# Optimization experiments

Measured on AMD Instinct MI355X. Metric: run time of the kernel, lower is better.

The kernel has to match this reference:

```python
import jax, jax.numpy as jnp
import numpy as np

D_MODEL = 1024
D_STATE = 16
EXPANSION = 2
GROUPS = 16
D_INNER = EXPANSION * D_MODEL          # 2048
GROUP_SIZE = D_INNER // GROUPS         # 128
B, T = 2, 1024


def _rmsnorm(x, g, eps=1e-6):
    return x * jax.lax.rsqrt(jnp.mean(x * x, axis=-1, keepdims=True) + eps) * g


def setup_inputs() -> dict:
    key = jax.random.key(0)
    ks = jax.random.split(key, 8)
    s_in = 1.0 / np.sqrt(D_MODEL)
    s_inner = 1.0 / np.sqrt(D_INNER)
    s_ff = 1.0 / np.sqrt(4 * D_MODEL)
    return {
        "x": jax.random.normal(ks[0], (B, T, D_MODEL), dtype=jnp.float32),
        "A_log": jnp.log(jnp.linspace(1.0, float(D_STATE), D_STATE)).astype(jnp.float32),
        "g1": jnp.ones((D_MODEL,), jnp.float32),
        "g2": jnp.ones((D_MODEL,), jnp.float32),
        "W_in": jax.random.normal(ks[1], (2 * D_INNER, D_MODEL), jnp.float32) * s_in,
        "W_param": jax.random.normal(ks[2], (GROUPS * (1 + 2 * D_STATE), D_INNER), jnp.float32) * s_inner,
        "W_out": jax.random.normal(ks[3], (D_MODEL, D_INNER), jnp.float32) * s_inner,
        "W_ffn1": jax.random.normal(ks[4], (4 * D_MODEL, D_MODEL), jnp.float32) * s_in,
        "b_ffn1": jnp.zeros((4 * D_MODEL,), jnp.float32),
        "W_ffn2": jax.random.normal(ks[5], (D_MODEL, 4 * D_MODEL), jnp.float32) * s_ff,
        "b_ffn2": jnp.zeros((D_MODEL,), jnp.float32),
    }


def _ssm(u, delta, b, c, A_log):
    # u,delta: [B,T,D]; b,c: [B,T,D,N]. Sequential recurrence equivalent to
    # the module's chunked cumprod/cumsum formulation.
    A = -jnp.exp(A_log)                                   # [N]
    deltaA = jnp.clip(delta[..., None] * A, -10.0, 10.0)  # [B,T,D,N]
    expA = jnp.exp(deltaA)
    frac_exact = (expA - 1.0) / (A + 1e-12)
    frac = jnp.where(jnp.abs(deltaA) < 1e-4, delta[..., None], frac_exact)
    Bu = frac * (b * u[..., None])                        # [B,T,D,N]

    def step(h, inp):
        Ah_t, Bu_t, c_t = inp                             # [B,D,N] each
        h = Ah_t * h + Bu_t
        return h, jnp.sum(h * c_t, axis=-1)               # y_t: [B,D]

    tm = lambda a: jnp.moveaxis(a, 1, 0)                  # time-major [T,B,D,N]
    h0 = jnp.zeros(u.shape[:1] + u.shape[2:] + (A.shape[0],), u.dtype)
    _, ys = jax.lax.scan(step, h0, (tm(expA), tm(Bu), tm(c)))
    return jnp.moveaxis(ys, 0, 1)                         # [B,T,D]


def reference(x, A_log, g1, g2, W_in, W_param, W_out, W_ffn1, b_ffn1, W_ffn2, b_ffn2):
    Bsz, Tlen, _ = x.shape
    z = _rmsnorm(x, g1)
    xz_gate = jnp.einsum('btd,ed->bte', z, W_in)          # [B,T,2*D_inner]
    xz, gate = jnp.split(xz_gate, 2, axis=-1)
    xz = jax.nn.silu(xz)

    params = jnp.einsum('btd,pd->btp', xz, W_param)
    params = params.reshape(Bsz, Tlen, GROUPS, 1 + 2 * D_STATE)
    delta_g = params[..., :1]                             # [B,T,G,1]
    b_g = params[..., 1:1 + D_STATE]                      # [B,T,G,N]
    c_g = params[..., 1 + D_STATE:]                       # [B,T,G,N]
    delta = jax.nn.softplus(jnp.repeat(delta_g[..., 0], GROUP_SIZE, axis=2))  # [B,T,D_inner]
    b = jnp.repeat(b_g, GROUP_SIZE, axis=2)               # [B,T,D_inner,N]
    c = jnp.repeat(c_g, GROUP_SIZE, axis=2)

    y_ssm = _ssm(xz, delta, b, c, A_log)                  # [B,T,D_inner]
    y = y_ssm * jax.nn.silu(gate)
    y = jnp.einsum('bte,de->btd', y, W_out)
    x = x + y                                             # residual (dropout/droppath = identity in eval)

    h2 = _rmsnorm(x, g2)
    ffn = jnp.einsum('btf,df->btd',
                     jax.nn.silu(jnp.einsum('btd,fd->btf', h2, W_ffn1) + b_ffn1),
                     W_ffn2) + b_ffn2
    return x + ffn
```

## Files before the change

kernel.cpp:

```cpp
#include <hip/hip_runtime.h>
#include <hip/hip_bf16.h>
#include <stdint.h>

#define ROWS 2048
#define DM   1024
#define DI   2048
#define PPAD 640

typedef __bf16 bf16_t;
typedef __attribute__((ext_vector_type(8))) __bf16 bf16x8;
typedef __attribute__((ext_vector_type(4))) __bf16 bf16x4;
typedef __attribute__((ext_vector_type(4))) float f32x4;
typedef __attribute__((address_space(1))) void gvoid_t;
typedef __attribute__((address_space(3))) void lvoid_t;

#define G_IN   1048576ll
#define G_PAR  327680ll
#define G_OUT  524288ll
#define G_F1   1048576ll
#define G_F2   1048576ll
__global__ __launch_bounds__(256) void cvt_all(const float* __restrict__ W_in,
                                               const float* __restrict__ W_param,
                                               const float* __restrict__ W_out,
                                               const float* __restrict__ W_f1,
                                               const float* __restrict__ W_f2,
                                               bf16_t* o_in, bf16_t* o_par,
                                               bf16_t* o_out, bf16_t* o_f1,
                                               bf16_t* o_f2) {
  int64_t g4 = (int64_t)blockIdx.x * 256 + threadIdx.x;
  const float* src; bf16_t* dst; int64_t e;
  if (g4 < G_IN) { e = g4 * 4; src = W_in; dst = o_in; }
  else if (g4 < G_IN + G_PAR) {
    e = (g4 - G_IN) * 4;
    int row = (int)(e >> 11), col = (int)(e & 2047);
    float4 v = make_float4(0.f, 0.f, 0.f, 0.f);
    if (row < 528) v = *(const float4*)(W_param + (int64_t)row * 2048 + col);
    bf16_t* o = o_par + e;
    o[0] = (bf16_t)v.x; o[1] = (bf16_t)v.y; o[2] = (bf16_t)v.z; o[3] = (bf16_t)v.w;
    return;
  }
  else if (g4 < G_IN + G_PAR + G_OUT) { e = (g4 - G_IN - G_PAR) * 4; src = W_out; dst = o_out; }
  else if (g4 < G_IN + G_PAR + G_OUT + G_F1) { e = (g4 - G_IN - G_PAR - G_OUT) * 4; src = W_f1; dst = o_f1; }
  else { e = (g4 - G_IN - G_PAR - G_OUT - G_F1) * 4; src = W_f2; dst = o_f2; }
  float4 v = *(const float4*)(src + e);
  bf16_t* o = dst + e;
  o[0] = (bf16_t)v.x; o[1] = (bf16_t)v.y; o[2] = (bf16_t)v.z; o[3] = (bf16_t)v.w;
}

__global__ __launch_bounds__(256) void rmsnorm_k(const float* __restrict__ x,
                                                 const float* __restrict__ g,
                                                 bf16_t* __restrict__ out) {
  int row = blockIdx.x;
  int tid = threadIdx.x;
  const float4 v = *(const float4*)(x + (int64_t)row * DM + tid * 4);
  float ss = v.x * v.x + v.y * v.y + v.z * v.z + v.w * v.w;
#pragma unroll
  for (int o = 32; o; o >>= 1) ss += __shfl_xor(ss, o, 64);
  __shared__ float red[4];
  if ((tid & 63) == 0) red[tid >> 6] = ss;
  __syncthreads();
  float tot = red[0] + red[1] + red[2] + red[3];
  float sc = rsqrtf(tot * (1.0f / DM) + 1e-6f);
  const float4 gv = *(const float4*)(g + tid * 4);
  bf16_t* o = out + (int64_t)row * DM + tid * 4;
  o[0] = (bf16_t)(v.x * sc * gv.x);
  o[1] = (bf16_t)(v.y * sc * gv.y);
  o[2] = (bf16_t)(v.z * sc * gv.z);
  o[3] = (bf16_t)(v.w * sc * gv.w);
}

__global__ __launch_bounds__(256) void silu_cvt(const float* __restrict__ in,
                                                bf16_t* __restrict__ out,
                                                int in_stride, int ncols) {
  int64_t e = ((int64_t)blockIdx.x * 256 + threadIdx.x) * 4;
  int row = (int)(e / ncols);
  int col = (int)(e % ncols);
  const float4 v = *(const float4*)(in + (int64_t)row * in_stride + col);
  bf16_t* o = out + e;
  o[0] = (bf16_t)(v.x / (1.f + expf(-v.x)));
  o[1] = (bf16_t)(v.y / (1.f + expf(-v.y)));
  o[2] = (bf16_t)(v.z / (1.f + expf(-v.z)));
  o[3] = (bf16_t)(v.w / (1.f + expf(-v.w)));
}

__global__ __launch_bounds__(256) void ssm_prep(const float* __restrict__ params,
                                                const float* __restrict__ A_log,
                                                float* __restrict__ ssmp, int nparts) {
  int gid = blockIdx.x * 256 + threadIdx.x;
  int bg = gid >> 10, t = gid & 1023;
  int b = bg >> 4, g = bg & 15;
  float acc[33];
#pragma unroll
  for (int i = 0; i < 33; ++i) acc[i] = 0.f;
  for (int p = 0; p < nparts; ++p) {
    const float* pr = params + (int64_t)p * ROWS * PPAD + (int64_t)(b * 1024 + t) * PPAD + g * 33;
#pragma unroll
    for (int i = 0; i < 33; ++i) acc[i] += pr[i];
  }
  float raw = acc[0];
  float delta = raw > 0.f ? raw + log1pf(expf(-raw)) : log1pf(expf(raw));
  float* o = ssmp + (int64_t)gid * 48;
#pragma unroll
  for (int s = 0; s < 16; ++s) {
    float A = -expf(A_log[s]);
    float dA = delta * A;
    dA = fminf(10.f, fmaxf(-10.f, dA));
    float e = expf(dA);
    float frac = (fabsf(dA) < 1e-4f) ? delta : (e - 1.f) / (A + 1e-12f);
    o[s] = dA;
    o[16 + s] = frac * acc[1 + s];
    o[32 + s] = acc[17 + s];
  }
}

__global__ __launch_bounds__(256) void reduce_rms(const bf16_t* __restrict__ P,
                                                  const float* __restrict__ x,
                                                  const float* __restrict__ g,
                                                  float* __restrict__ xmid,
                                                  bf16_t* __restrict__ zb) {
  int row = blockIdx.x;
  int tid = threadIdx.x;
  int64_t base = (int64_t)row * DM + tid * 4;
  float4 v = *(const float4*)(x + base);
#pragma unroll
  for (int p = 0; p < 4; ++p) {
    bf16x4 pv = *(const bf16x4*)(P + (int64_t)p * ROWS * DM + base);
    v.x += (float)pv[0]; v.y += (float)pv[1]; v.z += (float)pv[2]; v.w += (float)pv[3];
  }
  *(float4*)(xmid + base) = v;
  float ss = v.x * v.x + v.y * v.y + v.z * v.z + v.w * v.w;
#pragma unroll
  for (int o = 32; o; o >>= 1) ss += __shfl_xor(ss, o, 64);
  __shared__ float red[4];
  if ((tid & 63) == 0) red[tid >> 6] = ss;
  __syncthreads();
  float tot = red[0] + red[1] + red[2] + red[3];
  float sc = rsqrtf(tot * (1.0f / DM) + 1e-6f);
  const float4 gv = *(const float4*)(g + tid * 4);
  bf16_t* o = zb + base;
  o[0] = (bf16_t)(v.x * sc * gv.x);
  o[1] = (bf16_t)(v.y * sc * gv.y);
  o[2] = (bf16_t)(v.z * sc * gv.z);
  o[3] = (bf16_t)(v.w * sc * gv.w);
}

__global__ __launch_bounds__(256) void reduce_bias(const bf16_t* __restrict__ P,
                                                   const float* __restrict__ res,
                                                   const float* __restrict__ bias,
                                                   float* __restrict__ out) {
  int64_t e = ((int64_t)blockIdx.x * 256 + threadIdx.x) * 4;
  int col = (int)(e % DM);
  float4 v = *(const float4*)(res + e);
  const float4 bv = *(const float4*)(bias + col);
  v.x += bv.x; v.y += bv.y; v.z += bv.z; v.w += bv.w;
#pragma unroll
  for (int p = 0; p < 4; ++p) {
    bf16x4 pv = *(const bf16x4*)(P + (int64_t)p * ROWS * DM + e);
    v.x += (float)pv[0]; v.y += (float)pv[1]; v.z += (float)pv[2]; v.w += (float)pv[3];
  }
  *(float4*)(out + e) = v;
}


__global__ __launch_bounds__(256) void ssm_chunk(const float* __restrict__ ssmp,
                                                 const bf16_t* __restrict__ u,
                                                 float* __restrict__ S,
                                                 float* __restrict__ Etot) {
  __shared__ __align__(16) float cf[64 * 48];
  __shared__ __align__(16) float Lb[64 * 16];
  __shared__ __align__(16) bf16_t wl[16 * 64];
  __shared__ __align__(16) bf16_t Ut[128 * 64];
  int bgc = blockIdx.x;
  int bg = bgc >> 4, c = bgc & 15;
  int b = bg >> 4, g = bg & 15;
  int t0 = c * 64;
  int tid = threadIdx.x;
  {
    const float4* src = (const float4*)(ssmp + ((int64_t)bg * 1024 + t0) * 48);
    float4* dst = (float4*)cf;
#pragma unroll
    for (int i = 0; i < 3; ++i) dst[i * 256 + tid] = src[i * 256 + tid];
  }
  {
    int lt = tid >> 4;
    int c8 = (tid & 15) * 8;
#pragma unroll
    for (int p = 0; p < 4; ++p) {
      int t = p * 16 + lt;
      bf16x8 v = *(const bf16x8*)(u + ((int64_t)(b * 1024) + t0 + t) * 2048 + g * 128 + c8);
#pragma unroll
      for (int j = 0; j < 8; ++j)
        Ut[(c8 + j) * 64 + (((t >> 3) ^ j) << 3) + (t & 7)] = v[j];
    }
  }
  __syncthreads();
  if (tid < 16) {
    float l = 0.f;
    for (int t = 0; t < 64; ++t) { l += cf[t * 48 + tid]; Lb[t * 16 + tid] = l; }
  }
  __syncthreads();
  {
    int s = tid >> 4, tb4 = (tid & 15) * 4;
    float lend = Lb[63 * 16 + s];
    bf16x4 wv;
#pragma unroll
    for (int j = 0; j < 4; ++j) {
      int t = tb4 + j;
      wv[j] = (bf16_t)(__expf(lend - Lb[t * 16 + s]) * cf[t * 48 + 16 + s]);
    }
    unsigned byo = (unsigned)(s * 128 + tb4 * 2) ^ ((unsigned)(s & 7) << 4);
    *(bf16x4*)((char*)wl + byo) = wv;
    if (tid < 16) Etot[(int64_t)bgc * 16 + tid] = __expf(Lb[63 * 16 + tid]);
  }
  __syncthreads();
  {
    int lane = tid & 63, wave = tid >> 6;
    int fr = lane & 15, kq = lane >> 4;
    f32x4 acc2[2] = {};
#pragma unroll
    for (int kk = 0; kk < 2; ++kk) {
      int kb = kk * 4 + kq;
      bf16x8 af = *(const bf16x8*)((const char*)wl +
                    ((unsigned)(fr * 128 + kb * 16) ^ ((unsigned)(fr & 7) << 4)));
#pragma unroll
      for (int q = 0; q < 2; ++q) {
        int ch = (wave * 2 + q) * 16 + fr;
        bf16x8 bfr = *(const bf16x8*)((const char*)Ut +
                       ((unsigned)(ch * 128 + kb * 16) ^ ((unsigned)(ch & 7) << 4)));
        acc2[q] = __builtin_amdgcn_mfma_f32_16x16x32_bf16(af, bfr, acc2[q], 0, 0, 0);
      }
    }
    float* Sp = S + (int64_t)bgc * 2048;
#pragma unroll
    for (int q = 0; q < 2; ++q) {
      int ch = (wave * 2 + q) * 16 + fr;
#pragma unroll
      for (int j = 0; j < 4; ++j) Sp[(kq * 4 + j) * 128 + ch] = acc2[q][j];
    }
  }
}

__global__ __launch_bounds__(256) void ssm_combine(const float* __restrict__ S,
                                                   const float* __restrict__ Etot,
                                                   float* __restrict__ H) {
  int gid = blockIdx.x * 256 + threadIdx.x;
  int bg = gid >> 11;
  int s = (gid >> 7) & 15;
  int ch = gid & 127;
  float h = 0.f;
  for (int c = 0; c < 16; ++c) {
    int bgc = bg * 16 + c;
    int64_t idx = ((int64_t)bgc * 16 + s) * 128 + ch;
    H[idx] = h;
    h = Etot[(int64_t)bgc * 16 + s] * h + S[idx];
  }
}

template <int GM>
__global__ __launch_bounds__(256) void ssm_out(const float* __restrict__ ssmp,
                                               const bf16_t* __restrict__ u,
                                               const float* __restrict__ H,
                                               const float* __restrict__ gate_f,
                                               const bf16_t* __restrict__ gate_b,
                                               int gstride,
                                               bf16_t* __restrict__ yout) {
  __shared__ __align__(16) float cf[64 * 48];
  __shared__ __align__(16) float Lb[64 * 16];
  __shared__ __align__(16) bf16_t Km[64 * 64];
  __shared__ __align__(16) bf16_t Ut[128 * 64];
  __shared__ __align__(16) bf16_t Hb[128 * 32];
  int bgc = blockIdx.x;
  int bg = bgc >> 4, c = bgc & 15;
  int b = bg >> 4, g = bg & 15;
  int t0 = c * 64;
  int tid = threadIdx.x;
  int lane = tid & 63, wave = tid >> 6;
  {
    const float4* src = (const float4*)(ssmp + ((int64_t)bg * 1024 + t0) * 48);
    float4* dst = (float4*)cf;
#pragma unroll
    for (int i = 0; i < 3; ++i) dst[i * 256 + tid] = src[i * 256 + tid];
  }
  {
    int lt = tid >> 4;
    int c8 = (tid & 15) * 8;
#pragma unroll
    for (int p = 0; p < 4; ++p) {
      int t = p * 16 + lt;
      bf16x8 v = *(const bf16x8*)(u + ((int64_t)(b * 1024) + t0 + t) * 2048 + g * 128 + c8);
#pragma unroll
      for (int j = 0; j < 8; ++j)
        Ut[(c8 + j) * 64 + (((t >> 3) ^ j) << 3) + (t & 7)] = v[j];
    }
  }
  {
    int ch = tid >> 1, h8 = (tid & 1) * 8;
    const float* Hp = H + (int64_t)bgc * 2048 + ch;
#pragma unroll
    for (int j = 0; j < 8; ++j) {
      Hb[ch * 32 + h8 + j] = (bf16_t)Hp[(h8 + j) * 128];
      Hb[ch * 32 + 16 + h8 + j] = (bf16_t)0.f;
    }
  }
  __syncthreads();
  if (tid < 16) {
    float l = 0.f;
    for (int t = 0; t < 64; ++t) { l += cf[t * 48 + tid]; Lb[t * 16 + tid] = l; }
  }
  __syncthreads();
  {
    int t = tid >> 2, tp0 = (tid & 3) * 16;
    float4 cv[4], lv[4];
#pragma unroll
    for (int i = 0; i < 4; ++i) {
      cv[i] = *(const float4*)&cf[t * 48 + 32 + i * 4];
      lv[i] = *(const float4*)&Lb[t * 16 + i * 4];
    }
    float kv[16];
#pragma unroll
    for (int i = 0; i < 16; ++i) {
      int tp = tp0 + i;
      float k = 0.f;
      if (tp <= t) {
#pragma unroll
        for (int q = 0; q < 4; ++q) {
          float4 lpv = *(const float4*)&Lb[tp * 16 + q * 4];
          float4 fbv = *(const float4*)&cf[tp * 48 + 16 + q * 4];
          k += cv[q].x * __expf(lv[q].x - lpv.x) * fbv.x
             + cv[q].y * __expf(lv[q].y - lpv.y) * fbv.y
             + cv[q].z * __expf(lv[q].z - lpv.z) * fbv.z
             + cv[q].w * __expf(lv[q].w - lpv.w) * fbv.w;
        }
      }
      kv[i] = k;
    }
    bf16x8 lo, hi;
#pragma unroll
    for (int i = 0; i < 8; ++i) { lo[i] = (bf16_t)kv[i]; hi[i] = (bf16_t)kv[8 + i]; }
    unsigned b0 = (unsigned)(t * 128 + tp0 * 2) ^ ((unsigned)(t & 7) << 4);
    unsigned b1 = (unsigned)(t * 128 + tp0 * 2 + 16) ^ ((unsigned)(t & 7) << 4);
    *(bf16x8*)((char*)Km + b0) = lo;
    *(bf16x8*)((char*)Km + b1) = hi;
  }
  __syncthreads();
  int fr = lane & 15, kq = lane >> 4;
  int trow = (wave >> 1) * 32, wc = (wave & 1) * 64;
  f32x4 acc[2][4] = {};
#pragma unroll
  for (int kk = 0; kk < 2; ++kk) {
    int kb = kk * 4 + kq;
    bf16x8 af[2];
#pragma unroll
    for (int mi = 0; mi < 2; ++mi) {
      int row = trow + mi * 16 + fr;
      af[mi] = *(const bf16x8*)((const char*)Km +
                 ((unsigned)(row * 128 + kb * 16) ^ ((unsigned)(row & 7) << 4)));
    }
#pragma unroll
    for (int ni = 0; ni < 4; ++ni) {
      int ch = wc + ni * 16 + fr;
      bf16x8 bfr = *(const bf16x8*)((const char*)Ut +
                     ((unsigned)(ch * 128 + kb * 16) ^ ((unsigned)(ch & 7) << 4)));
#pragma unroll
      for (int mi = 0; mi < 2; ++mi)
        acc[mi][ni] = __builtin_amdgcn_mfma_f32_16x16x32_bf16(af[mi], bfr, acc[mi][ni], 0, 0, 0);
    }
  }
  {
    int s0 = kq * 8;
    bf16x8 cef[2];
    if (s0 < 16) {
#pragma unroll
      for (int mi = 0; mi < 2; ++mi) {
        int t = trow + mi * 16 + fr;
#pragma unroll
        for (int j = 0; j < 8; ++j)
          cef[mi][j] = (bf16_t)(cf[t * 48 + 32 + s0 + j] * __expf(Lb[t * 16 + s0 + j]));
      }
    } else {
#pragma unroll
      for (int mi = 0; mi < 2; ++mi)
#pragma unroll
        for (int j = 0; j < 8; ++j) cef[mi][j] = (bf16_t)0.f;
    }
#pragma unroll
    for (int ni = 0; ni < 4; ++ni) {
      int ch = wc + ni * 16 + fr;
      bf16x8 bhf = *(const bf16x8*)((const char*)Hb + ch * 64 + s0 * 2);
#pragma unroll
      for (int mi = 0; mi < 2; ++mi)
        acc[mi][ni] = __builtin_amdgcn_mfma_f32_16x16x32_bf16(cef[mi], bhf, acc[mi][ni], 0, 0, 0);
    }
  }
  {
    int64_t rowbase = (int64_t)b * 1024 + t0;
    int colbase = g * 128;
#pragma unroll
    for (int mi = 0; mi < 2; ++mi) {
#pragma unroll
      for (int ni = 0; ni < 4; ++ni) {
        int col = colbase + wc + ni * 16 + fr;
#pragma unroll
        for (int j = 0; j < 4; ++j) {
          int t = trow + mi * 16 + kq * 4 + j;
          float sg;
          if (GM) {
            sg = (float)gate_b[(rowbase + t) * 2048 + col];
          } else {
            float gv = gate_f[(rowbase + t) * (int64_t)gstride + col];
            sg = gv / (1.f + __expf(-gv));
          }
          yout[(rowbase + t) * 2048 + col] = (bf16_t)(acc[mi][ni][j] * sg);
        }
      }
    }
  }
}

template <int EPI>
__device__ __forceinline__ void epi_store(float v, int64_t r, int64_t cn, int N,
                                          float* Cz, const float* bias,
                                          const float* res, bf16_t* obf,
                                          bf16_t* ogate, int z) {
  if (EPI & 1) v += bias[cn];
  if (EPI & 2) v += res[r * N + cn];
  if (EPI & 4) {
    float sv = v / (1.f + __expf(-v));
    if (cn < 2048) obf[r * 2048 + cn] = (bf16_t)sv;
    else ogate[r * 2048 + cn - 2048] = (bf16_t)sv;
  } else if (EPI & 8) {
    obf[r * N + cn] = (bf16_t)(v / (1.f + __expf(-v)));
  } else if (EPI & 16) {
    obf[(int64_t)z * ROWS * N + r * N + cn] = (bf16_t)v;
  } else {
    Cz[r * N + cn] = v;
  }
}

template <int EPI>
__global__ __launch_bounds__(256) void gemm_bt(const bf16_t* __restrict__ A,
                                               const bf16_t* __restrict__ Bw,
                                               float* __restrict__ C,
                                               const float* __restrict__ bias,
                                               const float* __restrict__ res,
                                               bf16_t* __restrict__ obf,
                                               bf16_t* __restrict__ ogate,
                                               int N, int Kps) {
  __shared__ bf16_t As[2][128 * 64];
  __shared__ bf16_t Bs[2][128 * 64];
  const int tid = threadIdx.x;
  const int wave = tid >> 6;
  const int lane = tid & 63;
  const int64_t m0 = (int64_t)blockIdx.y * 128;
  const int64_t n0 = (int64_t)blockIdx.x * 128;
  const int K = Kps * gridDim.z;
  const int kbeg = blockIdx.z * Kps;
  float* Cz = C + (int64_t)blockIdx.z * ROWS * N;
  const int wm = (wave >> 1) * 64;
  const int wn = (wave & 1) * 64;
  f32x4 acc[4][4] = {};

  const int er = tid >> 3;
  const int ec = (tid * 8) & 63;
  const int fr = lane & 15;
  const int kq = (lane >> 4) * 8;

  auto stage = [&](int buf, int k0) {
#pragma unroll
    for (int i = 0; i < 4; ++i) {
      const bf16_t* ga = A + (m0 + er + i * 32) * K + k0 + ec;
      __builtin_amdgcn_global_load_lds((gvoid_t*)ga,
                                       (lvoid_t*)&As[buf][(i * 256 + wave * 64) * 8],
                                       16, 0, 0);
    }
#pragma unroll
    for (int i = 0; i < 4; ++i) {
      const bf16_t* gb = Bw + (n0 + er + i * 32) * K + k0 + ec;
      __builtin_amdgcn_global_load_lds((gvoid_t*)gb,
                                       (lvoid_t*)&Bs[buf][(i * 256 + wave * 64) * 8],
                                       16, 0, 0);
    }
  };
  auto compute = [&](int buf) {
#pragma unroll
    for (int kk = 0; kk < 2; ++kk) {
      bf16x8 af[4], bv[4];
#pragma unroll
      for (int mi = 0; mi < 4; ++mi)
        af[mi] = *reinterpret_cast<const bf16x8*>(&As[buf][(wm + mi * 16 + fr) * 64 + kk * 32 + kq]);
#pragma unroll
      for (int ni = 0; ni < 4; ++ni)
        bv[ni] = *reinterpret_cast<const bf16x8*>(&Bs[buf][(wn + ni * 16 + fr) * 64 + kk * 32 + kq]);
#pragma unroll
      for (int mi = 0; mi < 4; ++mi)
#pragma unroll
        for (int ni = 0; ni < 4; ++ni)
          acc[mi][ni] = __builtin_amdgcn_mfma_f32_16x16x32_bf16(af[mi], bv[ni], acc[mi][ni], 0, 0, 0);
    }
  };

  const int nk = Kps >> 6;
  stage(0, kbeg);
  asm volatile("s_waitcnt vmcnt(0)" ::: "memory");
  __builtin_amdgcn_s_barrier();
  int kc = kbeg;
  for (int t = 0; t < nk; t += 2) {
    stage(1, kc + 64);
    compute(0);
    asm volatile("s_waitcnt vmcnt(0)" ::: "memory");
    __builtin_amdgcn_s_barrier();
    if (t + 2 < nk) stage(0, kc + 128);
    compute(1);
    asm volatile("s_waitcnt vmcnt(0)" ::: "memory");
    __builtin_amdgcn_s_barrier();
    kc += 128;
  }

  const int crow = (lane >> 4) * 4;
  const int ccol = lane & 15;
#pragma unroll
  for (int mi = 0; mi < 4; ++mi)
#pragma unroll
    for (int ni = 0; ni < 4; ++ni)
#pragma unroll
      for (int j = 0; j < 4; ++j)
        epi_store<EPI>(acc[mi][ni][j], m0 + wm + mi * 16 + crow + j,
                       n0 + wn + ni * 16 + ccol, N, Cz, bias, res, obf, ogate,
                       blockIdx.z);
}

template <int EPI>
__global__ __launch_bounds__(512, 2) void gemm_big(const bf16_t* __restrict__ A,
                                                   const bf16_t* __restrict__ Bw,
                                                   float* __restrict__ C,
                                                   const float* __restrict__ bias,
                                                   const float* __restrict__ res,
                                                   bf16_t* __restrict__ obf,
                                                   bf16_t* __restrict__ ogate,
                                                   int N, int Kps) {
  __shared__ bf16_t As[2][128 * 64];
  __shared__ bf16_t Bs[2][256 * 64];
  const int tid = threadIdx.x;
  const int wave = tid >> 6;
  const int lane = tid & 63;
  const int64_t m0 = (int64_t)blockIdx.y * 128;
  const int64_t n0 = (int64_t)blockIdx.x * 256;
  const int K = Kps * gridDim.z;
  const int kbeg = blockIdx.z * Kps;
  float* Cz = C + (int64_t)blockIdx.z * ROWS * N;
  const int wm = (wave >> 2) * 64;
  const int wc = (wave & 3) * 64;
  const int fr = lane & 15;
  const int kq16 = (lane >> 4) * 16;
  const int er = tid >> 3;
  const int ec_sw = ((tid & 7) * 8) ^ ((er & 7) << 3);
  f32x4 acc[4][4] = {};

  auto stage = [&](int buf, int k0) {
#pragma unroll
    for (int i = 0; i < 2; ++i) {
      const bf16_t* ga = A + (m0 + er + i * 64) * K + k0 + ec_sw;
      __builtin_amdgcn_global_load_lds((gvoid_t*)ga,
          (lvoid_t*)((char*)&As[buf][0] + i * 8192 + wave * 1024), 16, 0, 0);
    }
#pragma unroll
    for (int i = 0; i < 4; ++i) {
      const bf16_t* gb = Bw + (n0 + er + i * 64) * K + k0 + ec_sw;
      __builtin_amdgcn_global_load_lds((gvoid_t*)gb,
          (lvoid_t*)((char*)&Bs[buf][0] + i * 8192 + wave * 1024), 16, 0, 0);
    }
  };

  const int nk = Kps >> 6;
  stage(0, kbeg);
  if (nk > 1) {
    stage(1, kbeg + 64);
    asm volatile("s_waitcnt vmcnt(6)" ::: "memory");
  } else {
    asm volatile("s_waitcnt vmcnt(0)" ::: "memory");
  }
  __builtin_amdgcn_s_barrier();
  __builtin_amdgcn_sched_barrier(0);

  for (int t = 0; t < nk; ++t) {
    const int buf = t & 1;
    bf16x8 af[2][4], bf[2][4];
#pragma unroll
    for (int kk = 0; kk < 2; ++kk) {
#pragma unroll
      for (int mi = 0; mi < 4; ++mi) {
        int r = wm + mi * 16 + fr;
        af[kk][mi] = *(const bf16x8*)((const char*)&As[buf][0] + r * 128 +
                       ((kk * 64 + kq16) ^ ((r & 7) << 4)));
      }
#pragma unroll
      for (int ni = 0; ni < 4; ++ni) {
        int r = wc + ni * 16 + fr;
        bf[kk][ni] = *(const bf16x8*)((const char*)&Bs[buf][0] + r * 128 +
                       ((kk * 64 + kq16) ^ ((r & 7) << 4)));
      }
    }
    asm volatile("s_waitcnt lgkmcnt(0)" ::: "memory");
    __builtin_amdgcn_sched_barrier(0);
    __builtin_amdgcn_s_barrier();
    __builtin_amdgcn_sched_barrier(0);
    if (t + 2 < nk) stage(buf, kbeg + (t + 2) * 64);
    __builtin_amdgcn_s_setprio(1);
#pragma unroll
    for (int kk = 0; kk < 2; ++kk)
#pragma unroll
      for (int mi = 0; mi < 4; ++mi)
#pragma unroll
        for (int ni = 0; ni < 4; ++ni)
          acc[mi][ni] = __builtin_amdgcn_mfma_f32_16x16x32_bf16(
              af[kk][mi], bf[kk][ni], acc[mi][ni], 0, 0, 0);
    __builtin_amdgcn_s_setprio(0);
    if (t + 1 < nk) {
      if (t + 2 < nk) asm volatile("s_waitcnt vmcnt(6)" ::: "memory");
      else            asm volatile("s_waitcnt vmcnt(0)" ::: "memory");
      __builtin_amdgcn_s_barrier();
      __builtin_amdgcn_sched_barrier(0);
    }
  }

  const int crow = (lane >> 4) * 4;
  const int ccol = lane & 15;
#pragma unroll
  for (int mi = 0; mi < 4; ++mi)
#pragma unroll
    for (int ni = 0; ni < 4; ++ni)
#pragma unroll
      for (int j = 0; j < 4; ++j)
        epi_store<EPI>(acc[mi][ni][j], m0 + wm + mi * 16 + crow + j,
                       n0 + wc + ni * 16 + ccol, N, Cz, bias, res, obf, ogate,
                       blockIdx.z);
}

extern "C" void kernel_launch(void* const* d_in, const int* in_sizes, int n_in,
                              void* d_out, int out_size, void* d_ws, size_t ws_size,
                              hipStream_t stream) {
  const float* x       = (const float*)d_in[0];
  const float* A_log   = (const float*)d_in[1];
  const float* g1      = (const float*)d_in[2];
  const float* g2      = (const float*)d_in[3];
  const float* W_in    = (const float*)d_in[4];
  const float* W_param = (const float*)d_in[5];
  const float* W_out   = (const float*)d_in[6];
  const float* W_ffn1  = (const float*)d_in[7];
  const float* b_ffn1  = (const float*)d_in[8];
  const float* W_ffn2  = (const float*)d_in[9];
  const float* b_ffn2  = (const float*)d_in[10];
  float* out = (float*)d_out;

  char* ws = (char*)d_ws;
  size_t off = 0;
  auto alloc = [&](size_t bytes) {
    char* p = ws + off;
    off += (bytes + 255) & ~(size_t)255;
    return p;
  };
  bf16_t* wb_in  = (bf16_t*)alloc(4096ull * 1024 * 2);
  bf16_t* wb_par = (bf16_t*)alloc((size_t)PPAD * 2048 * 2);
  bf16_t* wb_out = (bf16_t*)alloc(1024ull * 2048 * 2);
  bf16_t* wb_f1  = (bf16_t*)alloc(4096ull * 1024 * 2);
  bf16_t* wb_f2  = (bf16_t*)alloc(1024ull * 4096 * 2);
  bf16_t* zbuf   = (bf16_t*)alloc(2048ull * 1024 * 2);
  float*  xzg    = (float*)alloc(2048ull * 4096 * 4);
  float*  params = (float*)alloc(2048ull * PPAD * 4);
  float*  ssmp   = (float*)alloc(32ull * 1024 * 48 * 4);
  float*  xmid   = (float*)alloc(2048ull * 1024 * 4);
  char*   regA   = alloc(2048ull * 4096 * 2);
  bf16_t* xz_act = (bf16_t*)regA;
  bf16_t* y_b16  = (bf16_t*)(regA + 2048ull * 2048 * 2);
  bf16_t* f_act  = (bf16_t*)regA;
  bf16_t* sgate  = (bf16_t*)xzg;
  float* Sbuf = params;
  float* Etot = params + 32ull * 16 * 16 * 128;
  float* Hbuf = xmid;
  float*  psum = (float*)alloc(4ull * ROWS * 1024 * 4);
  bf16_t* pb16 = (bf16_t*)psum;
  const bool sk = (off <= ws_size);

  dim3 b256(256), b512(512);
  cvt_all<<<15616, b256, 0, stream>>>(W_in, W_param, W_out, W_ffn1, W_ffn2,
                                      wb_in, wb_par, wb_out, wb_f1, wb_f2);
  rmsnorm_k<<<2048, b256, 0, stream>>>(x, g1, zbuf);

  if (sk) {
    gemm_big<4><<<dim3(16, 16), b512, 0, stream>>>(zbuf, wb_in, psum, nullptr, nullptr, xz_act, sgate, 4096, 1024);
    gemm_bt<0><<<dim3(PPAD / 128, 16, 4), b256, 0, stream>>>(xz_act, wb_par, psum, nullptr, nullptr, nullptr, nullptr, PPAD, 512);
    ssm_prep<<<128, b256, 0, stream>>>(psum, A_log, ssmp, 4);
    ssm_chunk<<<512, b256, 0, stream>>>(ssmp, xz_act, Sbuf, Etot);
    ssm_combine<<<256, b256, 0, stream>>>(Sbuf, Etot, Hbuf);
    ssm_out<1><<<512, b256, 0, stream>>>(ssmp, xz_act, Hbuf, nullptr, sgate, 2048, y_b16);
    gemm_big<16><<<dim3(4, 16, 4), b512, 0, stream>>>(y_b16, wb_out, psum, nullptr, nullptr, pb16, nullptr, 1024, 512);
    reduce_rms<<<2048, b256, 0, stream>>>(pb16, x, g2, xmid, zbuf);
    gemm_big<9><<<dim3(16, 16), b512, 0, stream>>>(zbuf, wb_f1, psum, b_ffn1, nullptr, f_act, nullptr, 4096, 1024);
    gemm_big<16><<<dim3(4, 16, 4), b512, 0, stream>>>(f_act, wb_f2, psum, nullptr, nullptr, pb16, nullptr, 1024, 1024);
    reduce_bias<<<2048, b256, 0, stream>>>(pb16, xmid, b_ffn2, out);
  } else {
    gemm_bt<0><<<dim3(32, 16), b256, 0, stream>>>(zbuf, wb_in, xzg, nullptr, nullptr, nullptr, nullptr, 4096, 1024);
    silu_cvt<<<4096, b256, 0, stream>>>(xzg, xz_act, 4096, 2048);
    gemm_bt<0><<<dim3(PPAD / 128, 16), b256, 0, stream>>>(xz_act, wb_par, params, nullptr, nullptr, nullptr, nullptr, PPAD, 2048);
    ssm_prep<<<128, b256, 0, stream>>>(params, A_log, ssmp, 1);
    ssm_chunk<<<512, b256, 0, stream>>>(ssmp, xz_act, Sbuf, Etot);
    ssm_combine<<<256, b256, 0, stream>>>(Sbuf, Etot, Hbuf);
    ssm_out<0><<<512, b256, 0, stream>>>(ssmp, xz_act, Hbuf, xzg + 2048, nullptr, 4096, y_b16);
    gemm_bt<2><<<dim3(8, 16), b256, 0, stream>>>(y_b16, wb_out, xmid, nullptr, x, nullptr, nullptr, 1024, 2048);
    rmsnorm_k<<<2048, b256, 0, stream>>>(xmid, g2, zbuf);
    gemm_bt<1><<<dim3(32, 16), b256, 0, stream>>>(zbuf, wb_f1, xzg, b_ffn1, nullptr, nullptr, nullptr, 4096, 1024);
    silu_cvt<<<8192, b256, 0, stream>>>(xzg, f_act, 4096, 4096);
    gemm_bt<3><<<dim3(8, 16), b256, 0, stream>>>(f_act, wb_f2, out, b_ffn2, xmid, nullptr, nullptr, 1024, 4096);
  }
}
```

Baseline: 194.2 us.

## Fuse weight conversion with RMSNorm, add XCD swizzle, split MFMA phases, bf16 partials

The weight-conversion kernel and the first RMSNorm are merged into one launch by appending 2048 norm blocks to the conversion grid. Both GEMM kernels remap block indices with an XCD-aware swizzle so neighbouring tiles land on the same chiplet and share L2. In gemm_big, the first k-slice of MFMAs now issues after a partial LDS wait, before the barrier, to overlap math with the remaining LDS reads. The W_param split-K partials are written as bf16 instead of fp32 to cut traffic into ssm_prep, which costs some precision in the delta, B and C parameters.

Result: faster. 188.6 us (-2.9%).

```diff
diff --git a/kernel.cpp b/kernel.cpp
--- a/kernel.cpp
+++ b/kernel.cpp
@@ -19,14 +19,38 @@
 #define G_OUT  524288ll
 #define G_F1   1048576ll
 #define G_F2   1048576ll
-__global__ __launch_bounds__(256) void cvt_all(const float* __restrict__ W_in,
-                                               const float* __restrict__ W_param,
-                                               const float* __restrict__ W_out,
-                                               const float* __restrict__ W_f1,
-                                               const float* __restrict__ W_f2,
-                                               bf16_t* o_in, bf16_t* o_par,
-                                               bf16_t* o_out, bf16_t* o_f1,
-                                               bf16_t* o_f2) {
+#define CVT_BLOCKS 15616
+__global__ __launch_bounds__(256) void prep0(const float* __restrict__ W_in,
+                                             const float* __restrict__ W_param,
+                                             const float* __restrict__ W_out,
+                                             const float* __restrict__ W_f1,
+                                             const float* __restrict__ W_f2,
+                                             bf16_t* o_in, bf16_t* o_par,
+                                             bf16_t* o_out, bf16_t* o_f1,
+                                             bf16_t* o_f2,
+                                             const float* __restrict__ x,
+                                             const float* __restrict__ g1,
+                                             bf16_t* __restrict__ zb) {
+  if (blockIdx.x >= CVT_BLOCKS) {
+    int row = blockIdx.x - CVT_BLOCKS;
+    int tid = threadIdx.x;
+    const float4 v = *(const float4*)(x + (int64_t)row * DM + tid * 4);
+    float ss = v.x * v.x + v.y * v.y + v.z * v.z + v.w * v.w;
+#pragma unroll
+    for (int o = 32; o; o >>= 1) ss += __shfl_xor(ss, o, 64);
+    __shared__ float red[4];
+    if ((tid & 63) == 0) red[tid >> 6] = ss;
+    __syncthreads();
+    float tot = red[0] + red[1] + red[2] + red[3];
+    float sc = rsqrtf(tot * (1.0f / DM) + 1e-6f);
+    const float4 gv = *(const float4*)(g1 + tid * 4);
+    bf16_t* o = zb + (int64_t)row * DM + tid * 4;
+    o[0] = (bf16_t)(v.x * sc * gv.x);
+    o[1] = (bf16_t)(v.y * sc * gv.y);
+    o[2] = (bf16_t)(v.z * sc * gv.z);
+    o[3] = (bf16_t)(v.w * sc * gv.w);
+    return;
+  }
   int64_t g4 = (int64_t)blockIdx.x * 256 + threadIdx.x;
   const float* src; bf16_t* dst; int64_t e;
   if (g4 < G_IN) { e = g4 * 4; src = W_in; dst = o_in; }
@@ -83,7 +107,8 @@
   o[3] = (bf16_t)(v.w / (1.f + expf(-v.w)));
 }
 
-__global__ __launch_bounds__(256) void ssm_prep(const float* __restrict__ params,
+template <typename T>
+__global__ __launch_bounds__(256) void ssm_prep(const T* __restrict__ params,
                                                 const float* __restrict__ A_log,
                                                 float* __restrict__ ssmp, int nparts) {
   int gid = blockIdx.x * 256 + threadIdx.x;
@@ -93,9 +118,9 @@
 #pragma unroll
   for (int i = 0; i < 33; ++i) acc[i] = 0.f;
   for (int p = 0; p < nparts; ++p) {
-    const float* pr = params + (int64_t)p * ROWS * PPAD + (int64_t)(b * 1024 + t) * PPAD + g * 33;
-#pragma unroll
-    for (int i = 0; i < 33; ++i) acc[i] += pr[i];
+    const T* pr = params + (int64_t)p * ROWS * PPAD + (int64_t)(b * 1024 + t) * PPAD + g * 33;
+#pragma unroll
+    for (int i = 0; i < 33; ++i) acc[i] += (float)pr[i];
   }
   float raw = acc[0];
   float delta = raw > 0.f ? raw + log1pf(expf(-raw)) : log1pf(expf(raw));
@@ -437,6 +462,18 @@
   }
 }
 
+__device__ __forceinline__ void xcd_swz(int& bx, int& by, int& bz) {
+  int gx = gridDim.x, gy = gridDim.y, gz = gridDim.z;
+  int flat = blockIdx.x + gx * (blockIdx.y + gy * blockIdx.z);
+  int nwg = gx * gy * gz;
+  int swz = flat;
+  if ((nwg & 7) == 0) swz = (flat & 7) * (nwg >> 3) + (flat >> 3);
+  bx = swz % gx;
+  int rem = swz / gx;
+  by = rem % gy;
+  bz = rem / gy;
+}
+
 template <int EPI>
 __global__ __launch_bounds__(256) void gemm_bt(const bf16_t* __restrict__ A,
                                                const bf16_t* __restrict__ Bw,
@@ -451,11 +488,13 @@
   const int tid = threadIdx.x;
   const int wave = tid >> 6;
   const int lane = tid & 63;
-  const int64_t m0 = (int64_t)blockIdx.y * 128;
-  const int64_t n0 = (int64_t)blockIdx.x * 128;
+  int bxi, byi, bzi;
+  xcd_swz(bxi, byi, bzi);
+  const int64_t m0 = (int64_t)byi * 128;
+  const int64_t n0 = (int64_t)bxi * 128;
   const int K = Kps * gridDim.z;
-  const int kbeg = blockIdx.z * Kps;
-  float* Cz = C + (int64_t)blockIdx.z * ROWS * N;
+  const int kbeg = bzi * Kps;
+  float* Cz = C + (int64_t)bzi * ROWS * N;
   const int wm = (wave >> 1) * 64;
   const int wn = (wave & 1) * 64;
   f32x4 acc[4][4] = {};
@@ -526,7 +565,7 @@
       for (int j = 0; j < 4; ++j)
         epi_store<EPI>(acc[mi][ni][j], m0 + wm + mi * 16 + crow + j,
                        n0 + wn + ni * 16 + ccol, N, Cz, bias, res, obf, ogate,
-                       blockIdx.z);
+                       bzi);
 }
 
 template <int EPI>
@@ -543,11 +582,13 @@
   const int tid = threadIdx.x;
   const int wave = tid >> 6;
   const int lane = tid & 63;
-  const int64_t m0 = (int64_t)blockIdx.y * 128;
-  const int64_t n0 = (int64_t)blockIdx.x * 256;
+  int bxi, byi, bzi;
+  xcd_swz(bxi, byi, bzi);
+  const int64_t m0 = (int64_t)byi * 128;
+  const int64_t n0 = (int64_t)bxi * 256;
   const int K = Kps * gridDim.z;
-  const int kbeg = blockIdx.z * Kps;
-  float* Cz = C + (int64_t)blockIdx.z * ROWS * N;
+  const int kbeg = bzi * Kps;
+  float* Cz = C + (int64_t)bzi * ROWS * N;
   const int wm = (wave >> 2) * 64;
   const int wc = (wave & 3) * 64;
   const int fr = lane & 15;
@@ -600,6 +641,17 @@
                        ((kk * 64 + kq16) ^ ((r & 7) << 4)));
       }
     }
+    asm volatile("s_waitcnt lgkmcnt(8)" ::: "memory");
+    __builtin_amdgcn_sched_barrier(0);
+    __builtin_amdgcn_s_setprio(1);
+#pragma unroll
+    for (int mi = 0; mi < 4; ++mi)
+#pragma unroll
+      for (int ni = 0; ni < 4; ++ni)
+        acc[mi][ni] = __builtin_amdgcn_mfma_f32_16x16x32_bf16(
+            af[0][mi], bf[0][ni], acc[mi][ni], 0, 0, 0);
+    __builtin_amdgcn_s_setprio(0);
+    __builtin_amdgcn_sched_barrier(0);
     asm volatile("s_waitcnt lgkmcnt(0)" ::: "memory");
     __builtin_amdgcn_sched_barrier(0);
     __builtin_amdgcn_s_barrier();
@@ -607,13 +659,11 @@
     if (t + 2 < nk) stage(buf, kbeg + (t + 2) * 64);
     __builtin_amdgcn_s_setprio(1);
 #pragma unroll
-    for (int kk = 0; kk < 2; ++kk)
-#pragma unroll
-      for (int mi = 0; mi < 4; ++mi)
-#pragma unroll
-        for (int ni = 0; ni < 4; ++ni)
-          acc[mi][ni] = __builtin_amdgcn_mfma_f32_16x16x32_bf16(
-              af[kk][mi], bf[kk][ni], acc[mi][ni], 0, 0, 0);
+    for (int mi = 0; mi < 4; ++mi)
+#pragma unroll
+      for (int ni = 0; ni < 4; ++ni)
+        acc[mi][ni] = __builtin_amdgcn_mfma_f32_16x16x32_bf16(
+            af[1][mi], bf[1][ni], acc[mi][ni], 0, 0, 0);
     __builtin_amdgcn_s_setprio(0);
     if (t + 1 < nk) {
       if (t + 2 < nk) asm volatile("s_waitcnt vmcnt(6)" ::: "memory");
@@ -633,7 +683,7 @@
       for (int j = 0; j < 4; ++j)
         epi_store<EPI>(acc[mi][ni][j], m0 + wm + mi * 16 + crow + j,
                        n0 + wc + ni * 16 + ccol, N, Cz, bias, res, obf, ogate,
-                       blockIdx.z);
+                       bzi);
 }
 
 extern "C" void kernel_launch(void* const* d_in, const int* in_sizes, int n_in,
@@ -682,14 +732,14 @@
   const bool sk = (off <= ws_size);
 
   dim3 b256(256), b512(512);
-  cvt_all<<<15616, b256, 0, stream>>>(W_in, W_param, W_out, W_ffn1, W_ffn2,
-                                      wb_in, wb_par, wb_out, wb_f1, wb_f2);
-  rmsnorm_k<<<2048, b256, 0, stream>>>(x, g1, zbuf);
+  prep0<<<CVT_BLOCKS + 2048, b256, 0, stream>>>(W_in, W_param, W_out, W_ffn1, W_ffn2,
+                                                wb_in, wb_par, wb_out, wb_f1, wb_f2,
+                                                x, g1, zbuf);
 
   if (sk) {
     gemm_big<4><<<dim3(16, 16), b512, 0, stream>>>(zbuf, wb_in, psum, nullptr, nullptr, xz_act, sgate, 4096, 1024);
-    gemm_bt<0><<<dim3(PPAD / 128, 16, 4), b256, 0, stream>>>(xz_act, wb_par, psum, nullptr, nullptr, nullptr, nullptr, PPAD, 512);
-    ssm_prep<<<128, b256, 0, stream>>>(psum, A_log, ssmp, 4);
+    gemm_bt<16><<<dim3(PPAD / 128, 16, 4), b256, 0, stream>>>(xz_act, wb_par, psum, nullptr, nullptr, pb16, nullptr, PPAD, 512);
+    ssm_prep<bf16_t><<<128, b256, 0, stream>>>(pb16, A_log, ssmp, 4);
     ssm_chunk<<<512, b256, 0, stream>>>(ssmp, xz_act, Sbuf, Etot);
     ssm_combine<<<256, b256, 0, stream>>>(Sbuf, Etot, Hbuf);
     ssm_out<1><<<512, b256, 0, stream>>>(ssmp, xz_act, Hbuf, nullptr, sgate, 2048, y_b16);
@@ -702,7 +752,7 @@
     gemm_bt<0><<<dim3(32, 16), b256, 0, stream>>>(zbuf, wb_in, xzg, nullptr, nullptr, nullptr, nullptr, 4096, 1024);
     silu_cvt<<<4096, b256, 0, stream>>>(xzg, xz_act, 4096, 2048);
     gemm_bt<0><<<dim3(PPAD / 128, 16), b256, 0, stream>>>(xz_act, wb_par, params, nullptr, nullptr, nullptr, nullptr, PPAD, 2048);
-    ssm_prep<<<128, b256, 0, stream>>>(params, A_log, ssmp, 1);
+    ssm_prep<float><<<128, b256, 0, stream>>>(params, A_log, ssmp, 1);
     ssm_chunk<<<512, b256, 0, stream>>>(ssmp, xz_act, Sbuf, Etot);
     ssm_combine<<<256, b256, 0, stream>>>(Sbuf, Etot, Hbuf);
     ssm_out<0><<<512, b256, 0, stream>>>(ssmp, xz_act, Hbuf, xzg + 2048, nullptr, 4096, y_b16);
```
